# Kernel optimization log

Measured on AMD Instinct MI355X. Metric: run time of the kernel, lower is better.

The kernel has to match this reference:

```python
import jax, jax.numpy as jnp
import numpy as np
from jax import lax

B, T, D_LAT, D, H, J = 2048, 60, 100, 512, 256, 6
LRELU_SLOPE = 0.2
BN_EPS = 1e-5

# --- fixed kinematic-chain constants (stand-in for URDF: 6-DoF right arm) ---
AXES = np.array([[0,0,1],[1,0,0],[0,1,0],[1,0,0],[0,1,0],[1,0,0]], np.float32)
OFFS = np.array([[0,0,0.10],[0,0,0],[0,0,0],[0,-0.25,0],[0,0,0],[0,-0.25,0]], np.float32)
LOWER = np.array([-3.1416,-1.5708,-3.1416,-2.6,-1.5708,-1.2], np.float32)
UPPER = np.array([ 3.1416, 1.5708, 3.1416, 0.1, 1.5708, 1.2], np.float32)
FING1 = np.array([0.0,-0.08, 0.02], np.float32)
FING4 = np.array([0.0,-0.08,-0.02], np.float32)

def _skew(a):
    return np.array([[0,-a[2],a[1]],[a[2],0,-a[0]],[-a[1],a[0],0]], np.float32)

def fk_batch(joints):
    """joints: [B,T,6] normalized in [0,1]-ish -> poses [B,T,3,3]."""
    th = joints * (UPPER - LOWER) + LOWER                      # denormalize
    bt = th.shape[:2]
    R = jnp.broadcast_to(jnp.eye(3, dtype=th.dtype), bt + (3, 3))
    p = jnp.zeros(bt + (3,), th.dtype)
    pos = []
    for j in range(J):
        K = jnp.asarray(_skew(AXES[j]))
        a = th[..., j][..., None, None]
        Rj = jnp.eye(3, dtype=th.dtype) + jnp.sin(a) * K + (1.0 - jnp.cos(a)) * (K @ K)
        p = p + jnp.einsum('btij,j->bti', R, jnp.asarray(OFFS[j]))  # Trans then Rot
        R = jnp.einsum('btij,btjk->btik', R, Rj)
        pos.append(p)
    shoulder2, forearm, wrist = pos[1], pos[3], pos[5]
    f1 = wrist + jnp.einsum('btij,j->bti', R, jnp.asarray(FING1))
    f4 = wrist + jnp.einsum('btij,j->bti', R, jnp.asarray(FING4))
    body_L = (jnp.linalg.norm(shoulder2 - forearm, axis=-1)
              + jnp.linalg.norm(wrist - forearm, axis=-1)) * 0.5   # [B,T]
    rel = jnp.stack([wrist - shoulder2, f1 - shoulder2, f4 - shoulder2], axis=2)
    return rel / body_L[..., None, None]

def gru_dir(x, Wih, Whh, bih, bhh, reverse):
    xg = jnp.einsum('btd,gd->btg', x, Wih) + bih               # [B,T,3H]
    xg = jnp.swapaxes(xg, 0, 1)                                 # [T,B,3H]
    def step(h, g):
        gh = h @ Whh.T + bhh
        r = jax.nn.sigmoid(g[:, :H] + gh[:, :H])
        zz = jax.nn.sigmoid(g[:, H:2*H] + gh[:, H:2*H])
        n = jnp.tanh(g[:, 2*H:] + r * gh[:, 2*H:])
        hn = (1.0 - zz) * n + zz * h
        return hn, hn
    h0 = jnp.zeros((x.shape[0], H), x.dtype)
    _, ys = lax.scan(step, h0, xg, reverse=reverse)
    return jnp.swapaxes(ys, 0, 1)                               # [B,T,H]

def setup_inputs() -> dict:
    key = jax.random.key(0)
    ks = jax.random.split(key, 12)
    s = 0.05
    inp = {
        'z': jax.random.normal(ks[0], (B, D_LAT), jnp.float32),
        'W_fc': jax.random.normal(ks[1], (D, D_LAT), jnp.float32) * s,
        'b_fc': jnp.zeros((D,), jnp.float32),
        'bn_g': jnp.ones((D,), jnp.float32),
        'bn_b': jnp.zeros((D,), jnp.float32),
        'Wih_f': jax.random.normal(ks[2], (3*H, D), jnp.float32) * s,
        'Whh_f': jax.random.normal(ks[3], (3*H, H), jnp.float32) * s,
        'bih_f': jnp.zeros((3*H,), jnp.float32),
        'bhh_f': jnp.zeros((3*H,), jnp.float32),
        'Wih_b': jax.random.normal(ks[4], (3*H, D), jnp.float32) * s,
        'Whh_b': jax.random.normal(ks[5], (3*H, H), jnp.float32) * s,
        'bih_b': jnp.zeros((3*H,), jnp.float32),
        'bhh_b': jnp.zeros((3*H,), jnp.float32),
        'attn_W1': jax.random.normal(ks[6], (H, 2*H), jnp.float32) * s,
        'attn_b1': jnp.zeros((H,), jnp.float32),
        'attn_W2': jax.random.normal(ks[7], (H,), jnp.float32) * s,
        'joint_W': jax.random.normal(ks[8], (J, 2*H), jnp.float32) * s,
        'joint_b': jnp.zeros((J,), jnp.float32),
    }
    return inp

def reference(z, W_fc, b_fc, bn_g, bn_b, Wih_f, Whh_f, bih_f, bhh_f,
              Wih_b, Whh_b, bih_b, bhh_b, attn_W1, attn_b1, attn_W2,
              joint_W, joint_b):
    # fc: Linear + BatchNorm1d (training-mode batch stats) + LeakyReLU(0.2)
    h0 = z @ W_fc.T + b_fc                                      # [B,512]
    mu = jnp.mean(h0, axis=0)
    var = jnp.mean((h0 - mu) ** 2, axis=0)
    hb = (h0 - mu) * jax.lax.rsqrt(var + BN_EPS) * bn_g + bn_b
    h = jnp.where(hb >= 0, hb, LRELU_SLOPE * hb)
    x = jnp.broadcast_to(h[:, None, :], (h.shape[0], T, D))     # repeat over seq
    # bidirectional GRU
    gf = gru_dir(x, Wih_f, Whh_f, bih_f, bhh_f, False)
    gb = gru_dir(x, Wih_b, Whh_b, bih_b, bhh_b, True)
    gru_out = jnp.concatenate([gf, gb], axis=-1)                # [B,T,512]
    # attention over time
    a = jnp.tanh(jnp.einsum('btd,hd->bth', gru_out, attn_W1) + attn_b1)
    w = jax.nn.softmax(jnp.einsum('bth,h->bt', a, attn_W2), axis=1)[..., None]
    c = jnp.sum(w * gru_out, axis=1, keepdims=True)             # [B,1,512]
    joints = jnp.einsum('btd,jd->btj', gru_out + c, joint_W) + joint_b
    return fk_batch(joints)                                     # [B,T,3,3]
```

## Files before the change

kernel.cpp:

```cpp
#include <hip/hip_runtime.h>
#include <hip/hip_fp16.h>

#define NB 2048
#define NT 60
#define NDL 100
#define ND 512
#define NH 256
#define NG 768

#define L2E  1.44269504f
#define L2E2 2.88539008f

typedef const float* __restrict__ fpp;
typedef _Float16 half8 __attribute__((ext_vector_type(8)));
typedef float floatx4 __attribute__((ext_vector_type(4)));

__device__ __forceinline__ float fast_rcp(float x) {
  return __builtin_amdgcn_rcpf(x);
}
__device__ __forceinline__ float fast_exp2(float x) {
#if __has_builtin(__builtin_amdgcn_exp2f)
  return __builtin_amdgcn_exp2f(x);
#else
  return exp2f(x);
#endif
}
__device__ __forceinline__ float fsin(float x) {
#if __has_builtin(__builtin_amdgcn_sinf)
  return __builtin_amdgcn_sinf(x * 0.15915494309189535f);
#else
  return __sinf(x);
#endif
}
__device__ __forceinline__ float fcos(float x) {
#if __has_builtin(__builtin_amdgcn_cosf)
  return __builtin_amdgcn_cosf(x * 0.15915494309189535f);
#else
  return __cosf(x);
#endif
}

__global__ __launch_bounds__(256) void gemm_fc(
    fpp A, fpp Bm, fpp bias, float* __restrict__ C,
    int M, int N, int K, int lda, int ldb, int ldc)
{
  __shared__ float As[16][68];
  __shared__ float Bs[16][68];
  const int bm = blockIdx.x * 64, bn = blockIdx.y * 64;
  const int tid = threadIdx.x;
  const int tx = tid & 15, ty = tid >> 4;
  float acc[4][4] = {};
  for (int k0 = 0; k0 < K; k0 += 16) {
#pragma unroll
    for (int i = 0; i < 4; i++) {
      int e = tid + i * 256;
      int m = e >> 4, k = e & 15;
      As[k][m] = (k0 + k < K) ? A[(size_t)(bm + m) * lda + k0 + k] : 0.f;
      Bs[k][m] = (k0 + k < K) ? Bm[(size_t)(bn + m) * ldb + k0 + k] : 0.f;
    }
    __syncthreads();
#pragma unroll
    for (int kk = 0; kk < 16; kk++) {
      float4 av = *(const float4*)&As[kk][ty * 4];
      float4 bv = *(const float4*)&Bs[kk][tx * 4];
      float a_[4] = {av.x, av.y, av.z, av.w};
      float b_[4] = {bv.x, bv.y, bv.z, bv.w};
#pragma unroll
      for (int i = 0; i < 4; i++)
#pragma unroll
        for (int j = 0; j < 4; j++)
          acc[i][j] = fmaf(a_[i], b_[j], acc[i][j]);
    }
    __syncthreads();
  }
#pragma unroll
  for (int i = 0; i < 4; i++) {
    int m = bm + ty * 4 + i;
#pragma unroll
    for (int j = 0; j < 4; j++) {
      int n = bn + tx * 4 + j;
      C[(size_t)m * ldc + n] = acc[i][j] + bias[n];
    }
  }
}

__global__ __launch_bounds__(256) void bn_partial(
    const float* __restrict__ h0, float* __restrict__ s1g,
    float* __restrict__ s2g)
{
  const int r0 = blockIdx.x * 32;
  const int tid = threadIdx.x;
  float a1 = 0.f, a2 = 0.f, b1 = 0.f, b2 = 0.f;
  for (int r = 0; r < 32; r++) {
    float v = h0[(size_t)(r0 + r) * ND + tid];
    float w = h0[(size_t)(r0 + r) * ND + tid + 256];
    a1 += v; a2 += v * v;
    b1 += w; b2 += w * w;
  }
  atomicAdd(&s1g[tid], a1);
  atomicAdd(&s2g[tid], a2);
  atomicAdd(&s1g[tid + 256], b1);
  atomicAdd(&s2g[tid + 256], b2);
}

__global__ void bn_lrelu_h16(const float* __restrict__ h0,
                             fpp g, fpp b,
                             const float* __restrict__ s1g,
                             const float* __restrict__ s2g,
                             __half* __restrict__ h16g)
{
  int idx = blockIdx.x * 256 + threadIdx.x;
  int d = idx & (ND - 1);
  float mu = s1g[d] * (1.f / NB);
  float var = s2g[d] * (1.f / NB) - mu * mu;
  float sc = g[d] * rsqrtf(var + 1e-5f);
  float sh = b[d] - mu * sc;
  float v = h0[idx] * sc + sh;
  h16g[idx] = __float2half(v >= 0.f ? v : 0.2f * v);
}

__global__ void convert_w(fpp whf, fpp whb, fpp w1, fpp wif, fpp wib, fpp jw,
                          __half* __restrict__ o_whf, __half* __restrict__ o_whb,
                          __half* __restrict__ o_w1, __half* __restrict__ o_wif,
                          __half* __restrict__ o_wib, __half* __restrict__ o_jw)
{
  int idx = blockIdx.x * 256 + threadIdx.x;
  if (idx < 196608) {
    float s = ((idx >> 16) == 2) ? L2E2 : L2E;
    o_whf[idx] = __float2half(whf[idx] * s);
  } else if (idx < 393216) {
    int e = idx - 196608;
    float s = ((e >> 16) == 2) ? L2E2 : L2E;
    o_whb[e] = __float2half(whb[e] * s);
  } else if (idx < 524288) {
    int e = idx - 393216;
    o_w1[e] = __float2half(w1[e] * L2E2);
  } else if (idx < 917504) {
    int e = idx - 524288;
    float s = ((e >> 17) == 2) ? L2E2 : L2E;
    o_wif[e] = __float2half(wif[e] * s);
  } else if (idx < 1310720) {
    int e = idx - 917504;
    float s = ((e >> 17) == 2) ? L2E2 : L2E;
    o_wib[e] = __float2half(wib[e] * s);
  } else if (idx < 1318912) {
    int e = idx - 1310720;
    o_jw[e] = (e < 6 * ND) ? __float2half(jw[e]) : __float2half(0.f);
  }
}

__global__ __launch_bounds__(256) void gemm16_dual(
    const __half* __restrict__ A,
    const __half* __restrict__ B0, const __half* __restrict__ B1,
    fpp bias0, fpp bias1, float* __restrict__ C0, float* __restrict__ C1,
    int N, int K)
{
  const __half* __restrict__ Bm = blockIdx.z ? B1 : B0;
  fpp bias = blockIdx.z ? bias1 : bias0;
  float* __restrict__ C = blockIdx.z ? C1 : C0;

  __shared__ __half As[64 * 40];
  __shared__ __half Bs[64 * 40];
  const int bm = blockIdx.x * 64, bn = blockIdx.y * 64;
  const int tid = threadIdx.x;
  const int wave = tid >> 6, lane = tid & 63;
  const int lm = lane & 15, quad = lane >> 4;
  floatx4 acc[4];
#pragma unroll
  for (int nt = 0; nt < 4; nt++) acc[nt] = (floatx4){0.f, 0.f, 0.f, 0.f};

  const int row = tid >> 2, kc = tid & 3;
  for (int k0 = 0; k0 < K; k0 += 32) {
    __syncthreads();
    *(float4*)&As[row * 40 + kc * 8] =
      *(const float4*)&A[(size_t)(bm + row) * K + k0 + kc * 8];
    *(float4*)&Bs[row * 40 + kc * 8] =
      *(const float4*)&Bm[(size_t)(bn + row) * K + k0 + kc * 8];
    __syncthreads();
    half8 af = *(const half8*)&As[(wave * 16 + lm) * 40 + quad * 8];
#pragma unroll
    for (int nt = 0; nt < 4; nt++) {
      half8 bf = *(const half8*)&Bs[(nt * 16 + lm) * 40 + quad * 8];
      acc[nt] = __builtin_amdgcn_mfma_f32_16x16x32_f16(af, bf, acc[nt], 0, 0, 0);
    }
  }
#pragma unroll
  for (int nt = 0; nt < 4; nt++) {
    int n = bn + nt * 16 + lm;
    float bv = bias[n] * ((n < 2 * NH) ? L2E : L2E2);
#pragma unroll
    for (int r = 0; r < 4; r++) {
      int m = bm + wave * 16 + quad * 4 + r;
      C[(size_t)m * N + n] = acc[nt][r] + bv;
    }
  }
}

#define GATES(C) do {                                                        \
    _Pragma("unroll")                                                        \
    for (int r = 0; r < 4; r++) {                                            \
      float er = fast_exp2(-acc[0][C][r]);                                   \
      float rg = fast_rcp(1.f + er);                                         \
      float ez = fast_exp2(-acc[1][C][r]);                                   \
      float tt = fast_exp2(fmaf(rg, acc[2][C][r], xn4[C][r]));               \
      float dd = tt + 1.f;                                                   \
      float num = fmaf(tt, ez + hp[C][r], hp[C][r] - ez);                    \
      float den = fmaf(dd, ez, dd);                                          \
      float hv = num * fast_rcp(den);                                        \
      hp[C][r] = hv;                                                         \
      hCur[(quad * 4 + r) * 264 + (n0 + C * 16 + lm)] = __float2half(hv);    \
    }                                                                        \
  } while (0)

#define CHAIN(C) do {                                                        \
    half8 t6[3], t7[3];                                                      \
    _Pragma("unroll")                                                        \
    for (int g = 0; g < 3; g++) {                                            \
      const __half* wp = &wts[wb + (g * 4 + C * 2) * 512];                   \
      t6[g] = *(const half8*)wp;                                             \
      t7[g] = *(const half8*)(wp + 512);                                     \
    }                                                                        \
    _Pragma("unroll")                                                        \
    for (int kb = 0; kb < 6; kb++)                                           \
      _Pragma("unroll")                                                      \
      for (int g = 0; g < 3; g++)                                            \
        acc[g][C] = __builtin_amdgcn_mfma_f32_16x16x32_f16(                  \
            a[kb], __builtin_bit_cast(half8, breg[g][C][kb]), acc[g][C],     \
            0, 0, 0);                                                        \
    _Pragma("unroll")                                                        \
    for (int g = 0; g < 3; g++)                                              \
      acc[g][C] = __builtin_amdgcn_mfma_f32_16x16x32_f16(                    \
          a[6], t6[g], acc[g][C], 0, 0, 0);                                  \
    _Pragma("unroll")                                                        \
    for (int g = 0; g < 3; g++)                                              \
      acc[g][C] = __builtin_amdgcn_mfma_f32_16x16x32_f16(                    \
          a[7], t7[g], acc[g][C], 0, 0, 0);                                  \
  } while (0)

__global__ __launch_bounds__(512, 2) void gru_persistent(
    const float* __restrict__ xg_f, const float* __restrict__ xg_b,
    const __half* __restrict__ whh16_f, const __half* __restrict__ whh16_b,
    fpp bhh_f, fpp bhh_b, __half* __restrict__ seq)
{
  const int dir  = blockIdx.x & 1;
  const int tile = blockIdx.x >> 1;
  const int bm   = tile * 16;
  const float* __restrict__ xg = dir ? xg_b : xg_f;
  const __half* __restrict__ Whh = dir ? whh16_b : whh16_f;
  fpp bhh = dir ? bhh_b : bhh_f;
  const int dcol = dir * NH;
  const int tid = threadIdx.x;
  const int wave = tid >> 6, lane = tid & 63;
  const int lm = lane & 15, quad = lane >> 4;
  const int n0 = wave * 32;

  __shared__ __half h16s[2][16 * 264];
  __shared__ __half wts[96 * 512];

  floatx4 breg[3][2][6];
  {
    const __half* bp[3][2];
#pragma unroll
    for (int g = 0; g < 3; g++)
#pragma unroll
      for (int c = 0; c < 2; c++)
        bp[g][c] = Whh + (size_t)(g * NH + n0 + c * 16 + lm) * NH + quad * 8;

#pragma unroll
    for (int g = 0; g < 3; g++)
#pragma unroll
      for (int c = 0; c < 2; c++)
#pragma unroll
        for (int kb = 0; kb < 6; kb++)
          breg[g][c][kb] = *(const floatx4*)(bp[g][c] + kb * 32);
#pragma unroll
    for (int g = 0; g < 3; g++)
#pragma unroll
      for (int c = 0; c < 2; c++)
#pragma unroll
        for (int kb = 0; kb < 6; kb++)
          asm volatile("" : "+v"(breg[g][c][kb]));

#pragma unroll
    for (int g = 0; g < 3; g++)
#pragma unroll
      for (int c = 0; c < 2; c++)
#pragma unroll
        for (int k2 = 0; k2 < 2; k2++)
          *(float4*)&wts[(wave * 12 + g * 4 + c * 2 + k2) * 512 + lane * 8] =
            *(const float4*)(bp[g][c] + 192 + k2 * 32);
  }

  floatx4 xr4[2], xz4[2], xn4[2];
  float bn_[2];
#pragma unroll
  for (int c = 0; c < 2; c++) {
    int n = n0 + c * 16 + lm;
    float br = bhh[n] * L2E, bz = bhh[NH + n] * L2E;
    bn_[c] = bhh[2 * NH + n] * L2E2;
#pragma unroll
    for (int r = 0; r < 4; r++) {
      int m = bm + quad * 4 + r;
      const float* xp = xg + (size_t)m * NG + n;
      xr4[c][r] = xp[0] + br;
      xz4[c][r] = xp[NH] + bz;
      xn4[c][r] = xp[2 * NH];
    }
  }

  float hp[2][4];
#pragma unroll
  for (int c = 0; c < 2; c++)
#pragma unroll
    for (int r = 0; r < 4; r++) hp[c][r] = 0.f;

  const int arow = lm * 264 + quad * 8;
  const int cm = tid >> 5, cpart = tid & 31;
  const int wb = wave * 6144 + lane * 8;

  __half* seqp = seq + ((size_t)(bm + cm) * NT + (dir ? NT - 1 : 0)) * ND
                 + dcol + cpart * 8;
  const ptrdiff_t seqd = dir ? -(ptrdiff_t)ND : (ptrdiff_t)ND;

  for (int step = 0; step < NT; step++) {
    const int cur = step & 1, prv = cur ^ 1;
    __half* __restrict__ hCur = h16s[cur];
    const __half* __restrict__ hPrv = h16s[prv];
    floatx4 acc[3][2];
#pragma unroll
    for (int c = 0; c < 2; c++) {
      acc[0][c] = xr4[c];
      acc[1][c] = xz4[c];
      acc[2][c] = (floatx4){bn_[c], bn_[c], bn_[c], bn_[c]};
    }

    if (step > 0) {
      {
        float4 v = *(const float4*)&hPrv[cm * 264 + cpart * 8];
        *(float4*)seqp = v;
        seqp += seqd;
      }
      half8 a[8];
#pragma unroll
      for (int kb = 0; kb < 8; kb++)
        a[kb] = *(const half8*)&hPrv[arow + kb * 32];

      __builtin_amdgcn_s_setprio(1);
      CHAIN(0);
      __builtin_amdgcn_s_setprio(0);
      GATES(0);
      __builtin_amdgcn_s_setprio(1);
      CHAIN(1);
      __builtin_amdgcn_s_setprio(0);
      GATES(1);
    } else {
      GATES(0);
      GATES(1);
    }
    __syncthreads();
  }

  {
    const __half* hLast = h16s[(NT - 1) & 1];
    float4 v = *(const float4*)&hLast[cm * 264 + cpart * 8];
    *(float4*)seqp = v;
  }
}

__global__ __launch_bounds__(512, 4) void attn_score_mfma(
    const __half* __restrict__ seq, const __half* __restrict__ w116,
    const __half* __restrict__ jw16, fpp b1, fpp W2,
    float* __restrict__ scores, float* __restrict__ gJ)
{
  const int bm = blockIdx.x * 128;
  const int tid = threadIdx.x;
  const int wave = tid >> 6, lane = tid & 63;
  const int lm = lane & 15, quad = lane >> 4;
  const int mh = wave & 1;
  const int nh = wave >> 1;

  __shared__ __half As[128 * 40];
  __shared__ __half Bs[256 * 40];
  __shared__ __half Js[16 * 40];
  __shared__ float partial[4][128];

  floatx4 acc[4][4];
  floatx4 accJ[4];
#pragma unroll
  for (int t = 0; t < 4; t++) {
#pragma unroll
    for (int u = 0; u < 4; u++) acc[t][u] = (floatx4){0.f, 0.f, 0.f, 0.f};
    accJ[t] = (floatx4){0.f, 0.f, 0.f, 0.f};
  }

  const int srow = tid >> 2, skc8 = (tid & 3) * 8;

  for (int k0 = 0; k0 < ND; k0 += 32) {
    __syncthreads();
    *(float4*)&As[srow * 40 + skc8] =
      *(const float4*)&seq[(size_t)(bm + srow) * ND + k0 + skc8];
#pragma unroll
    for (int i = 0; i < 2; i++)
      *(float4*)&Bs[(srow + i * 128) * 40 + skc8] =
        *(const float4*)&w116[(size_t)(srow + i * 128) * ND + k0 + skc8];
    if (tid < 64)
      *(float4*)&Js[srow * 40 + skc8] =
        *(const float4*)&jw16[(size_t)srow * ND + k0 + skc8];
    __syncthreads();

    half8 a[4];
#pragma unroll
    for (int t = 0; t < 4; t++)
      a[t] = *(const half8*)&As[((mh * 4 + t) * 16 + lm) * 40 + quad * 8];
#pragma unroll
    for (int u = 0; u < 4; u++) {
      half8 bf = *(const half8*)&Bs[((nh * 4 + u) * 16 + lm) * 40 + quad * 8];
#pragma unroll
      for (int t = 0; t < 4; t++)
        acc[t][u] = __builtin_amdgcn_mfma_f32_16x16x32_f16(a[t], bf, acc[t][u], 0, 0, 0);
    }
    if (nh == 3) {
      half8 bj = *(const half8*)&Js[lm * 40 + quad * 8];
#pragma unroll
      for (int t = 0; t < 4; t++)
        accJ[t] = __builtin_amdgcn_mfma_f32_16x16x32_f16(a[t], bj, accJ[t], 0, 0, 0);
    }
  }

  float rs[4][4] = {};
#pragma unroll
  for (int u = 0; u < 4; u++) {
    int n = (nh * 4 + u) * 16 + lm;
    float b1v = b1[n] * L2E2, w2v = W2[n];
#pragma unroll
    for (int t = 0; t < 4; t++)
#pragma unroll
      for (int r = 0; r < 4; r++) {
        float tt = fast_exp2(acc[t][u][r] + b1v);
        float th = fmaf(-2.f, fast_rcp(tt + 1.f), 1.f);
        rs[t][r] = fmaf(th, w2v, rs[t][r]);
      }
  }
#pragma unroll
  for (int t = 0; t < 4; t++)
#pragma unroll
    for (int r = 0; r < 4; r++) {
      rs[t][r] += __shfl_xor(rs[t][r], 1);
      rs[t][r] += __shfl_xor(rs[t][r], 2);
      rs[t][r] += __shfl_xor(rs[t][r], 4);
      rs[t][r] += __shfl_xor(rs[t][r], 8);
    }
  if (lm == 0) {
#pragma unroll
    for (int t = 0; t < 4; t++)
#pragma unroll
      for (int r = 0; r < 4; r++)
        partial[nh][mh * 64 + t * 16 + quad * 4 + r] = rs[t][r];
  }
  if (nh == 3) {
#pragma unroll
    for (int t = 0; t < 4; t++)
#pragma unroll
      for (int r = 0; r < 4; r++) {
        int row = bm + mh * 64 + t * 16 + quad * 4 + r;
        gJ[(size_t)row * 16 + lm] = accJ[t][r];
      }
  }
  __syncthreads();
  if (tid < 128)
    scores[bm + tid] = partial[0][tid] + partial[1][tid] +
                       partial[2][tid] + partial[3][tid];
}

__constant__ float c_lower[6] = {-3.1416f, -1.5708f, -3.1416f, -2.6f, -1.5708f, -1.2f};
__constant__ float c_upper[6] = { 3.1416f,  1.5708f,  3.1416f,  0.1f,  1.5708f,  1.2f};

__global__ __launch_bounds__(64) void attn_post(
    const float* __restrict__ scores_in, const float* __restrict__ gJ,
    fpp jb, float* __restrict__ out)
{
  const int b = blockIdx.x;
  const int t = threadIdx.x;

  float v = (t < NT) ? scores_in[(size_t)b * NT + t] : -1e30f;
  float m = v;
#pragma unroll
  for (int off = 32; off >= 1; off >>= 1) m = fmaxf(m, __shfl_xor(m, off));
  float e = (t < NT) ? __expf(v - m) : 0.f;
  float sum = e;
#pragma unroll
  for (int off = 32; off >= 1; off >>= 1) sum += __shfl_xor(sum, off);
  float w = e * fast_rcp(sum);

  __shared__ float gj[NT * 16];
  __shared__ float wl[64];
  __shared__ float cj[16];
  wl[t] = w;
  const float* gsrc = gJ + (size_t)b * NT * 16;
#pragma unroll
  for (int i = 0; i < 15; i++) gj[t + i * 64] = gsrc[t + i * 64];
  __syncthreads();

  if (t < 16) {
    float s = 0.f;
    for (int tt = 0; tt < NT; tt++) s += wl[tt] * gj[tt * 16 + t];
    cj[t] = s;
  }
  __syncthreads();

  if (t >= NT) return;

  float th[6];
#pragma unroll
  for (int j = 0; j < 6; j++) {
    float jnt = gj[t * 16 + j] + cj[j] + jb[j];
    th[j] = jnt * (c_upper[j] - c_lower[j]) + c_lower[j];
  }

  float c0x = 1.f, c0y = 0.f, c0z = 0.f;
  float c1x = 0.f, c1y = 1.f, c1z = 0.f;
  float c2x = 0.f, c2y = 0.f, c2z = 1.f;
  float px = 0.f, py = 0.f, pz = 0.1f;
  float s, cc, tx_, ty_, tz_, ux_, uy_, uz_;

  s = fsin(th[0]); cc = fcos(th[0]);
  tx_ = cc * c0x + s * c1x; ty_ = cc * c0y + s * c1y; tz_ = cc * c0z + s * c1z;
  ux_ = -s * c0x + cc * c1x; uy_ = -s * c0y + cc * c1y; uz_ = -s * c0z + cc * c1z;
  c0x = tx_; c0y = ty_; c0z = tz_; c1x = ux_; c1y = uy_; c1z = uz_;

  float shx = px, shy = py, shz = pz;
  s = fsin(th[1]); cc = fcos(th[1]);
  tx_ = cc * c1x + s * c2x; ty_ = cc * c1y + s * c2y; tz_ = cc * c1z + s * c2z;
  ux_ = -s * c1x + cc * c2x; uy_ = -s * c1y + cc * c2y; uz_ = -s * c1z + cc * c2z;
  c1x = tx_; c1y = ty_; c1z = tz_; c2x = ux_; c2y = uy_; c2z = uz_;

  s = fsin(th[2]); cc = fcos(th[2]);
  tx_ = cc * c0x - s * c2x; ty_ = cc * c0y - s * c2y; tz_ = cc * c0z - s * c2z;
  ux_ = s * c0x + cc * c2x; uy_ = s * c0y + cc * c2y; uz_ = s * c0z + cc * c2z;
  c0x = tx_; c0y = ty_; c0z = tz_; c2x = ux_; c2y = uy_; c2z = uz_;

  px -= 0.25f * c1x; py -= 0.25f * c1y; pz -= 0.25f * c1z;
  float fox = px, foy = py, foz = pz;
  s = fsin(th[3]); cc = fcos(th[3]);
  tx_ = cc * c1x + s * c2x; ty_ = cc * c1y + s * c2y; tz_ = cc * c1z + s * c2z;
  ux_ = -s * c1x + cc * c2x; uy_ = -s * c1y + cc * c2y; uz_ = -s * c1z + cc * c2z;
  c1x = tx_; c1y = ty_; c1z = tz_; c2x = ux_; c2y = uy_; c2z = uz_;

  s = fsin(th[4]); cc = fcos(th[4]);
  tx_ = cc * c0x - s * c2x; ty_ = cc * c0y - s * c2y; tz_ = cc * c0z - s * c2z;
  ux_ = s * c0x + cc * c2x; uy_ = s * c0y + cc * c2y; uz_ = s * c0z + cc * c2z;
  c0x = tx_; c0y = ty_; c0z = tz_; c2x = ux_; c2y = uy_; c2z = uz_;

  px -= 0.25f * c1x; py -= 0.25f * c1y; pz -= 0.25f * c1z;
  float wx = px, wy = py, wz = pz;
  s = fsin(th[5]); cc = fcos(th[5]);
  tx_ = cc * c1x + s * c2x; ty_ = cc * c1y + s * c2y; tz_ = cc * c1z + s * c2z;
  ux_ = -s * c1x + cc * c2x; uy_ = -s * c1y + cc * c2y; uz_ = -s * c1z + cc * c2z;
  c1x = tx_; c1y = ty_; c1z = tz_; c2x = ux_; c2y = uy_; c2z = uz_;

  float f1x = wx - 0.08f * c1x + 0.02f * c2x;
  float f1y = wy - 0.08f * c1y + 0.02f * c2y;
  float f1z = wz - 0.08f * c1z + 0.02f * c2z;
  float f4x = wx - 0.08f * c1x - 0.02f * c2x;
  float f4y = wy - 0.08f * c1y - 0.02f * c2y;
  float f4z = wz - 0.08f * c1z - 0.02f * c2z;

  float dsx = shx - fox, dsy = shy - foy, dsz = shz - foz;
  float dwx = wx - fox, dwy = wy - foy, dwz = wz - foz;
  float bodyL = 0.5f * (sqrtf(dsx * dsx + dsy * dsy + dsz * dsz) +
                        sqrtf(dwx * dwx + dwy * dwy + dwz * dwz));
  float inv = fast_rcp(bodyL);

  float* o = out + ((size_t)b * NT + t) * 9;
  o[0] = (wx - shx) * inv; o[1] = (wy - shy) * inv; o[2] = (wz - shz) * inv;
  o[3] = (f1x - shx) * inv; o[4] = (f1y - shy) * inv; o[5] = (f1z - shz) * inv;
  o[6] = (f4x - shx) * inv; o[7] = (f4y - shy) * inv; o[8] = (f4z - shz) * inv;
}

extern "C" void kernel_launch(void* const* d_in, const int* in_sizes, int n_in,
                              void* d_out, int out_size, void* d_ws, size_t ws_size,
                              hipStream_t stream)
{
  fpp z     = (fpp)d_in[0];
  fpp W_fc  = (fpp)d_in[1];
  fpp b_fc  = (fpp)d_in[2];
  fpp bn_g  = (fpp)d_in[3];
  fpp bn_b  = (fpp)d_in[4];
  fpp Wih_f = (fpp)d_in[5];
  fpp Whh_f = (fpp)d_in[6];
  fpp bih_f = (fpp)d_in[7];
  fpp bhh_f = (fpp)d_in[8];
  fpp Wih_b = (fpp)d_in[9];
  fpp Whh_b = (fpp)d_in[10];
  fpp bih_b = (fpp)d_in[11];
  fpp bhh_b = (fpp)d_in[12];
  fpp aW1   = (fpp)d_in[13];
  fpp ab1   = (fpp)d_in[14];
  fpp aW2   = (fpp)d_in[15];
  fpp jW    = (fpp)d_in[16];
  fpp jb    = (fpp)d_in[17];

  float* ws     = (float*)d_ws;
  float* h0     = ws;
  float* xg_f   = h0 + 1048576;
  float* xg_b   = xg_f + 1572864;
  float* bns1   = xg_b + 1572864;
  float* bns2   = bns1 + 512;
  float* scores = bns2 + 512;
  float* cbuf   = scores + 122880;
  __half* gseq    = (__half*)(cbuf + 1048576);
  __half* whh16_f = gseq + 62914560;
  __half* whh16_b = whh16_f + 196608;
  __half* w116    = whh16_b + 196608;
  __half* wih16_f = w116 + 131072;
  __half* wih16_b = wih16_f + 393216;
  __half* h16g    = wih16_b + 393216;
  __half* jw16    = h16g + 1048576;
  float*  gJ      = (float*)(jw16 + 8192);

  convert_w<<<5152, 256, 0, stream>>>(Whh_f, Whh_b, aW1, Wih_f, Wih_b, jW,
                                      whh16_f, whh16_b, w116, wih16_f, wih16_b,
                                      jw16);
  hipMemsetAsync(bns1, 0, 1024 * sizeof(float), stream);
  gemm_fc<<<dim3(32, 8), 256, 0, stream>>>(z, W_fc, b_fc, h0,
                                           NB, ND, NDL, NDL, NDL, ND);
  bn_partial<<<64, 256, 0, stream>>>(h0, bns1, bns2);
  bn_lrelu_h16<<<4096, 256, 0, stream>>>(h0, bn_g, bn_b, bns1, bns2, h16g);
  gemm16_dual<<<dim3(32, 12, 2), 256, 0, stream>>>(
      h16g, wih16_f, wih16_b, bih_f, bih_b, xg_f, xg_b, NG, ND);
  gru_persistent<<<256, 512, 0, stream>>>(xg_f, xg_b, whh16_f, whh16_b,
                                          bhh_f, bhh_b, gseq);
  attn_score_mfma<<<960, 512, 0, stream>>>(gseq, w116, jw16, ab1, aW2,
                                           scores, gJ);
  attn_post<<<NB, 64, 0, stream>>>(scores, gJ, jb, (float*)d_out);
}
```

Before: 282.4 us.

## Double-buffer attention GEMM tiles, stagger GRU gate phases, widen BN partial grid

The attention-score kernel now double-buffers its A/B shared-memory tiles, using register prefetch of the next K-slice. This removes one barrier per iteration, and the joint-weight fragment is read straight from global memory instead of LDS. In the GRU persistent kernel, half the waves run the two chain/gate halves in swapped order so MFMA and transcendental work from different waves can overlap. The BN partial-reduction grid grows from 64 to 256 blocks, each handling 8 rows, at the cost of more atomics. The extra LDS buffer could reduce occupancy of the attention kernel.

New measurement: 307.0 us. +8.7%, slower.

```diff
diff --git a/kernel.cpp b/kernel.cpp
--- a/kernel.cpp
+++ b/kernel.cpp
@@ -88,10 +88,10 @@
     const float* __restrict__ h0, float* __restrict__ s1g,
     float* __restrict__ s2g)
 {
-  const int r0 = blockIdx.x * 32;
+  const int r0 = blockIdx.x * 8;
   const int tid = threadIdx.x;
   float a1 = 0.f, a2 = 0.f, b1 = 0.f, b2 = 0.f;
-  for (int r = 0; r < 32; r++) {
+  for (int r = 0; r < 8; r++) {
     float v = h0[(size_t)(r0 + r) * ND + tid];
     float w = h0[(size_t)(r0 + r) * ND + tid + 256];
     a1 += v; a2 += v * v;
@@ -253,6 +253,7 @@
   const int wave = tid >> 6, lane = tid & 63;
   const int lm = lane & 15, quad = lane >> 4;
   const int n0 = wave * 32;
+  const int ph = (wave >> 2) & 1;
 
   __shared__ __half h16s[2][16 * 264];
   __shared__ __half wts[96 * 512];
@@ -345,14 +346,25 @@
       for (int kb = 0; kb < 8; kb++)
         a[kb] = *(const half8*)&hPrv[arow + kb * 32];
 
-      __builtin_amdgcn_s_setprio(1);
-      CHAIN(0);
-      __builtin_amdgcn_s_setprio(0);
-      GATES(0);
-      __builtin_amdgcn_s_setprio(1);
-      CHAIN(1);
-      __builtin_amdgcn_s_setprio(0);
-      GATES(1);
+      if (ph == 0) {
+        __builtin_amdgcn_s_setprio(1);
+        CHAIN(0);
+        __builtin_amdgcn_s_setprio(0);
+        GATES(0);
+        __builtin_amdgcn_s_setprio(1);
+        CHAIN(1);
+        __builtin_amdgcn_s_setprio(0);
+        GATES(1);
+      } else {
+        __builtin_amdgcn_s_setprio(1);
+        CHAIN(1);
+        __builtin_amdgcn_s_setprio(0);
+        GATES(1);
+        __builtin_amdgcn_s_setprio(1);
+        CHAIN(0);
+        __builtin_amdgcn_s_setprio(0);
+        GATES(0);
+      }
     } else {
       GATES(0);
       GATES(1);
@@ -379,9 +391,8 @@
   const int mh = wave & 1;
   const int nh = wave >> 1;
 
-  __shared__ __half As[128 * 40];
-  __shared__ __half Bs[256 * 40];
-  __shared__ __half Js[16 * 40];
+  __shared__ __half As[2][128 * 40];
+  __shared__ __half Bs[2][256 * 40];
   __shared__ float partial[4][128];
 
   floatx4 acc[4][4];
@@ -394,37 +405,54 @@
   }
 
   const int srow = tid >> 2, skc8 = (tid & 3) * 8;
-
+  const __half* ap = &seq[(size_t)(bm + srow) * ND + skc8];
+  const __half* bp0 = &w116[(size_t)srow * ND + skc8];
+  const __half* bp1 = &w116[(size_t)(srow + 128) * ND + skc8];
+  const __half* jp = &jw16[(size_t)lm * ND + quad * 8];
+
+  float4 pa, pb[2];
+  pa = *(const float4*)ap;
+  pb[0] = *(const float4*)bp0;
+  pb[1] = *(const float4*)bp1;
+  *(float4*)&As[0][srow * 40 + skc8] = pa;
+  *(float4*)&Bs[0][srow * 40 + skc8] = pb[0];
+  *(float4*)&Bs[0][(srow + 128) * 40 + skc8] = pb[1];
+  __syncthreads();
+
+  int cur = 0;
   for (int k0 = 0; k0 < ND; k0 += 32) {
-    __syncthreads();
-    *(float4*)&As[srow * 40 + skc8] =
-      *(const float4*)&seq[(size_t)(bm + srow) * ND + k0 + skc8];
-#pragma unroll
-    for (int i = 0; i < 2; i++)
-      *(float4*)&Bs[(srow + i * 128) * 40 + skc8] =
-        *(const float4*)&w116[(size_t)(srow + i * 128) * ND + k0 + skc8];
-    if (tid < 64)
-      *(float4*)&Js[srow * 40 + skc8] =
-        *(const float4*)&jw16[(size_t)srow * ND + k0 + skc8];
-    __syncthreads();
+    const bool more = (k0 + 32 < ND);
+    if (more) {
+      pa = *(const float4*)(ap + k0 + 32);
+      pb[0] = *(const float4*)(bp0 + k0 + 32);
+      pb[1] = *(const float4*)(bp1 + k0 + 32);
+    }
 
     half8 a[4];
 #pragma unroll
     for (int t = 0; t < 4; t++)
-      a[t] = *(const half8*)&As[((mh * 4 + t) * 16 + lm) * 40 + quad * 8];
+      a[t] = *(const half8*)&As[cur][((mh * 4 + t) * 16 + lm) * 40 + quad * 8];
 #pragma unroll
     for (int u = 0; u < 4; u++) {
-      half8 bf = *(const half8*)&Bs[((nh * 4 + u) * 16 + lm) * 40 + quad * 8];
+      half8 bf = *(const half8*)&Bs[cur][((nh * 4 + u) * 16 + lm) * 40 + quad * 8];
 #pragma unroll
       for (int t = 0; t < 4; t++)
         acc[t][u] = __builtin_amdgcn_mfma_f32_16x16x32_f16(a[t], bf, acc[t][u], 0, 0, 0);
     }
     if (nh == 3) {
-      half8 bj = *(const half8*)&Js[lm * 40 + quad * 8];
+      half8 bj = *(const half8*)(jp + k0);
 #pragma unroll
       for (int t = 0; t < 4; t++)
         accJ[t] = __builtin_amdgcn_mfma_f32_16x16x32_f16(a[t], bj, accJ[t], 0, 0, 0);
     }
+
+    if (more) {
+      *(float4*)&As[cur ^ 1][srow * 40 + skc8] = pa;
+      *(float4*)&Bs[cur ^ 1][srow * 40 + skc8] = pb[0];
+      *(float4*)&Bs[cur ^ 1][(srow + 128) * 40 + skc8] = pb[1];
+      cur ^= 1;
+    }
+    __syncthreads();
   }
 
   float rs[4][4] = {};
@@ -624,7 +652,7 @@
   hipMemsetAsync(bns1, 0, 1024 * sizeof(float), stream);
   gemm_fc<<<dim3(32, 8), 256, 0, stream>>>(z, W_fc, b_fc, h0,
                                            NB, ND, NDL, NDL, NDL, ND);
-  bn_partial<<<64, 256, 0, stream>>>(h0, bns1, bns2);
+  bn_partial<<<256, 256, 0, stream>>>(h0, bns1, bns2);
   bn_lrelu_h16<<<4096, 256, 0, stream>>>(h0, bn_g, bn_b, bns1, bns2, h16g);
   gemm16_dual<<<dim3(32, 12, 2), 256, 0, stream>>>(
       h16g, wih16_f, wih16_b, bih_f, bih_b, xg_f, xg_b, NG, ND);
```
